# Performance work log

Measured on AMD Instinct MI355X. Metric: run time of the kernel, lower is better.

The kernel has to match this reference:

```python
import jax, jax.numpy as jnp
import numpy as np

N_HOSTS = 16
N_WINDOW = 3
GAT_IN = 3
D = 16          # d_model = gat_output_feats = n_hosts
NHEAD = 2
HD = D // NHEAD # 8
FF = 64
PROTO_DIM = 8
LATENT = N_HOSTS * D * N_WINDOW  # 768
LN_EPS = 1e-5


def _positional_encoding():
    pos = np.arange(N_WINDOW, dtype=np.float32)[:, None]
    div = np.exp(np.arange(0, D, 2, dtype=np.float32) * (-np.log(10000.0) / D))
    pe = np.zeros((N_WINDOW, D), dtype=np.float32)
    pe[:, 0::2] = np.sin(pos * div)
    pe[:, 1::2] = np.cos(pos * div)
    return jnp.asarray(pe[:, None, :])  # (n_window, 1, d_model)


def setup_inputs() -> dict:
    key = jax.random.key(0)
    ks = iter(jax.random.split(key, 40))
    p = lambda *s: jax.random.normal(next(ks), s, dtype=jnp.float32) * 0.05
    inp = {
        't': jax.random.normal(next(ks), (N_WINDOW * N_HOSTS * GAT_IN,), dtype=jnp.float32),
        's': jax.random.normal(next(ks), (N_HOSTS, PROTO_DIM), dtype=jnp.float32),
        # GAT (single head, fully connected 16-node graph)
        'gat_W': p(GAT_IN, D), 'gat_a_src': p(D), 'gat_a_dst': p(D),
        # time encoder Linear(16,16)
        'te_W': p(D, D), 'te_b': p(D),
        'pe': _positional_encoding(),
        # 2 transformer encoder layers, stacked on leading axis
        'qkv_W': p(2, 3 * D, D), 'qkv_b': p(2, 3 * D),
        'out_W': p(2, D, D), 'out_b': p(2, D),
        'ln1_g': jnp.ones((2, D), jnp.float32), 'ln1_b': jnp.zeros((2, D), jnp.float32),
        'ff1_W': p(2, FF, D), 'ff1_b': p(2, FF),
        'ff2_W': p(2, D, FF), 'ff2_b': p(2, D),
        'ln2_g': jnp.ones((2, D), jnp.float32), 'ln2_b': jnp.zeros((2, D), jnp.float32),
        # decoder heads
        'an_W': p(2 * N_HOSTS, LATENT), 'an_b': p(2 * N_HOSTS),
        'pr_W': p(PROTO_DIM * N_HOSTS, LATENT), 'pr_b': p(PROTO_DIM * N_HOSTS),
    }
    return inp


def _layer_norm(x, g, b):
    m = x.mean(-1, keepdims=True)
    v = ((x - m) ** 2).mean(-1, keepdims=True)
    return (x - m) * jax.lax.rsqrt(v + LN_EPS) * g + b


def reference(t, s, gat_W, gat_a_src, gat_a_dst, te_W, te_b, pe,
              qkv_W, qkv_b, out_W, out_b, ln1_g, ln1_b,
              ff1_W, ff1_b, ff2_W, ff2_b, ln2_g, ln2_b,
              an_W, an_b, pr_W, pr_b):
    # --- GAT over fully connected 16-host graph, per window ---
    x = t.reshape(N_WINDOW, N_HOSTS, GAT_IN)
    h = x @ gat_W                                   # (w, n, D)
    e_src = h @ gat_a_src                           # (w, n)
    e_dst = h @ gat_a_dst                           # (w, n)
    e = jax.nn.leaky_relu(e_src[:, :, None] + e_dst[:, None, :], 0.2)  # (w, src, dst)
    alpha = jax.nn.softmax(e, axis=1)               # softmax over sources, per dst
    gat_out = jax.nn.elu(jnp.einsum('wsd,wsf->wdf', alpha, h))         # (w, n, D)
    # --- time encode + positional encode (dropout = identity in eval) ---
    xe = gat_out @ te_W.T + te_b + pe               # (seq=3, batch=16, D)
    # --- 2 post-norm TransformerEncoderLayers ---
    inv_sqrt_hd = 1.0 / np.sqrt(HD).astype(np.float32)
    for l in range(2):
        qkv = xe @ qkv_W[l].T + qkv_b[l]            # (s, b, 3D)
        q, k, v = jnp.split(qkv, 3, axis=-1)
        hd = lambda z: z.reshape(N_WINDOW, N_HOSTS, NHEAD, HD).transpose(1, 2, 0, 3)  # (b,h,s,hd)
        q, k, v = hd(q), hd(k), hd(v)
        att = jax.nn.softmax(jnp.einsum('bhqd,bhkd->bhqk', q, k) * inv_sqrt_hd, axis=-1)
        ctx = jnp.einsum('bhqk,bhkd->bhqd', att, v).transpose(2, 0, 1, 3).reshape(N_WINDOW, N_HOSTS, D)
        xe = _layer_norm(xe + ctx @ out_W[l].T + out_b[l], ln1_g[l], ln1_b[l])
        ff = jax.nn.relu(xe @ ff1_W[l].T + ff1_b[l]) @ ff2_W[l].T + ff2_b[l]
        xe = _layer_norm(xe + ff, ln2_g[l], ln2_b[l])
    # --- flatten to latent (batch-major, matching permute(1,0,2).reshape) ---
    latent = xe.transpose(1, 0, 2).reshape(1, LATENT)
    # nn.LeakyReLU(True): negative_slope=True==1.0, i.e. identity (faithful to source)
    anomaly = jax.nn.leaky_relu(latent @ an_W.T + an_b, 1.0).reshape(N_HOSTS, 2)
    proto = jax.nn.sigmoid(latent @ pr_W.T + pr_b).reshape(N_HOSTS, PROTO_DIM)
    return anomaly, proto
```

## Files before the change

### kernel.cpp

```cpp
#include <hip/hip_runtime.h>
#include <hip/hip_bf16.h>


#define NW 3
#define NHOST 16
#define DM 16
#define FFD 64
#define LAT 768

typedef __hip_bfloat16 bf16;
typedef __attribute__((ext_vector_type(8))) unsigned short ushort8v;

static __device__ __forceinline__ float u2f(unsigned short u) {
    return __uint_as_float(((unsigned)u) << 16);
}

static __device__ __forceinline__ float lwf(const unsigned short* a, int i) { return u2f(a[i]); }
static __device__ __forceinline__ float lwf(const float* a, int i) { return a[i]; }

static __device__ __forceinline__ float gld(const bf16* p, int i) { return __bfloat162float(p[i]); }
static __device__ __forceinline__ float gld(const float* p, int i) { return p[i]; }
static __device__ __forceinline__ void gst(bf16* p, int i, float v) { p[i] = __float2bfloat16(v); }
static __device__ __forceinline__ void gst(float* p, int i, float v) { p[i] = v; }

enum {
    OFF_T    = 0,
    OFF_GATW = 144,
    OFF_ASRC = 192,
    OFF_ADST = 208,
    OFF_TEW  = 224,
    OFF_TEB  = 480,
    OFF_PE   = 496,
    OFF_QKVW = 544,
    OFF_QKVB = 2080,
    OFF_OUTW = 2176,
    OFF_OUTB = 2688,
    OFF_LN1G = 2720,
    OFF_LN1B = 2752,
    OFF_FF1W = 2784,
    OFF_FF1B = 4832,
    OFF_FF2W = 4960,
    OFF_FF2B = 7008,
    OFF_LN2G = 7040,
    OFF_LN2B = 7072,
    TOTAL_W  = 7104
};

struct Smem {
    float h[NW][NHOST][DM];
    float esrc[NW][NHOST];
    float edst[NW][NHOST];
    float alpha[NW][NHOST][NHOST];
    float xe[NW][NHOST][DM];
    float qkv[NW][NHOST][48];
    float ctx[NW][NHOST][DM];
    float tmp[NW][NHOST][DM];
    float ffh[NW][NHOST][FFD];
    float latent[LAT];
    float part[4];
};

template<typename T, typename WT>
__device__ void run_all(Smem& sm, WT* smW, int tid, int o,
    const T* t, const T* gat_W, const T* a_src, const T* a_dst,
    const T* te_W, const T* te_b, const T* pe,
    const T* qkv_W, const T* qkv_b, const T* out_W, const T* out_b,
    const T* ln1_g, const T* ln1_b,
    const T* ff1_W, const T* ff1_b, const T* ff2_W, const T* ff2_b,
    const T* ln2_g, const T* ln2_b,
    const T* an_W, const T* an_b, const T* pr_W, const T* pr_b,
    T* out)
{
    T wr0{}, wr1{}, wr2{}, wr3{};
    if (tid < 192) {
        const T* Wr = (o < 32) ? (an_W + o * LAT) : (pr_W + (o - 32) * LAT);
        wr0 = Wr[tid * 4];     wr1 = Wr[tid * 4 + 1];
        wr2 = Wr[tid * 4 + 2]; wr3 = Wr[tid * 4 + 3];
    }

    {
        constexpr int EPC = 16 / (int)sizeof(T);
        constexpr int NCHUNK = TOTAL_W / EPC;
        for (int g = tid; g < NCHUNK; g += 256) {
            int e = g * EPC;
            const T* p; int base;
            if      (e < OFF_GATW) { p = t;      base = OFF_T; }
            else if (e < OFF_ASRC) { p = gat_W;  base = OFF_GATW; }
            else if (e < OFF_ADST) { p = a_src;  base = OFF_ASRC; }
            else if (e < OFF_TEW)  { p = a_dst;  base = OFF_ADST; }
            else if (e < OFF_TEB)  { p = te_W;   base = OFF_TEW; }
            else if (e < OFF_PE)   { p = te_b;   base = OFF_TEB; }
            else if (e < OFF_QKVW) { p = pe;     base = OFF_PE; }
            else if (e < OFF_QKVB) { p = qkv_W;  base = OFF_QKVW; }
            else if (e < OFF_OUTW) { p = qkv_b;  base = OFF_QKVB; }
            else if (e < OFF_OUTB) { p = out_W;  base = OFF_OUTW; }
            else if (e < OFF_LN1G) { p = out_b;  base = OFF_OUTB; }
            else if (e < OFF_LN1B) { p = ln1_g;  base = OFF_LN1G; }
            else if (e < OFF_FF1W) { p = ln1_b;  base = OFF_LN1B; }
            else if (e < OFF_FF1B) { p = ff1_W;  base = OFF_FF1W; }
            else if (e < OFF_FF2W) { p = ff1_b;  base = OFF_FF1B; }
            else if (e < OFF_FF2B) { p = ff2_W;  base = OFF_FF2W; }
            else if (e < OFF_LN2G) { p = ff2_b;  base = OFF_FF2B; }
            else if (e < OFF_LN2B) { p = ln2_g;  base = OFF_LN2G; }
            else                   { p = ln2_b;  base = OFF_LN2B; }
            *(ushort8v*)((unsigned char*)smW + (size_t)e * sizeof(T)) =
                *(const ushort8v*)(p + (e - base));
        }
    }
    __syncthreads();

    for (int idx = tid; idx < NW * NHOST * DM; idx += 256) {
        int w = idx >> 8, r = idx & 255, n = r >> 4, f = r & 15;
        float acc = 0.f;
        #pragma unroll
        for (int i = 0; i < 3; ++i)
            acc += lwf(smW, OFF_T + (w * NHOST + n) * 3 + i) * lwf(smW, OFF_GATW + i * DM + f);
        sm.h[w][n][f] = acc;
    }
    __syncthreads();

    if (tid < 96) {
        int w = tid / 32, r = tid % 32, n = r & 15, which = r >> 4;
        int abase = which ? OFF_ADST : OFF_ASRC;
        float acc = 0.f;
        #pragma unroll
        for (int f = 0; f < DM; ++f) acc += sm.h[w][n][f] * lwf(smW, abase + f);
        if (which) sm.edst[w][n] = acc; else sm.esrc[w][n] = acc;
    }
    __syncthreads();

    if (tid < 48) {
        int w = tid / 16, d = tid & 15;
        float ed = sm.edst[w][d];
        float e[16];
        float mx = -1e30f;
        #pragma unroll
        for (int s = 0; s < 16; ++s) {
            float x = sm.esrc[w][s] + ed;
            x = x > 0.f ? x : 0.2f * x;
            e[s] = x;
            mx = fmaxf(mx, x);
        }
        float sum = 0.f;
        #pragma unroll
        for (int s = 0; s < 16; ++s) { e[s] = __expf(e[s] - mx); sum += e[s]; }
        float inv = 1.f / sum;
        #pragma unroll
        for (int s = 0; s < 16; ++s) sm.alpha[w][s][d] = e[s] * inv;
    }
    __syncthreads();

    for (int idx = tid; idx < NW * NHOST * DM; idx += 256) {
        int w = idx >> 8, r = idx & 255, d = r >> 4, f = r & 15;
        float acc = 0.f;
        #pragma unroll
        for (int s = 0; s < 16; ++s) acc += sm.alpha[w][s][d] * sm.h[w][s][f];
        sm.tmp[w][d][f] = acc > 0.f ? acc : (__expf(acc) - 1.f);
    }
    __syncthreads();

    for (int idx = tid; idx < NW * NHOST * DM; idx += 256) {
        int w = idx >> 8, r = idx & 255, n = r >> 4, f = r & 15;
        float acc = lwf(smW, OFF_TEB + f) + lwf(smW, OFF_PE + w * DM + f);
        #pragma unroll
        for (int g = 0; g < DM; ++g)
            acc += sm.tmp[w][n][g] * lwf(smW, OFF_TEW + f * DM + g);
        sm.xe[w][n][f] = acc;
    }
    __syncthreads();

    #pragma unroll 1
    for (int l = 0; l < 2; ++l) {
        int qW = OFF_QKVW + l * 768, qb = OFF_QKVB + l * 48;
        for (int idx = tid; idx < NW * NHOST * 48; idx += 256) {
            int w = idx / (NHOST * 48), r = idx % (NHOST * 48), n = r / 48, j = r % 48;
            float acc = lwf(smW, qb + j);
            #pragma unroll
            for (int f = 0; f < DM; ++f) acc += sm.xe[w][n][f] * lwf(smW, qW + j * DM + f);
            sm.qkv[w][n][j] = acc;
        }
        __syncthreads();

        if (tid < 96) {
            int b = tid / 6, r = tid % 6, hh = r / 3, qs = r % 3;
            const float inv_sqrt_hd = 0.35355339059327373f;
            float sc[3];
            #pragma unroll
            for (int ks = 0; ks < 3; ++ks) {
                float acc = 0.f;
                #pragma unroll
                for (int d0 = 0; d0 < 8; ++d0)
                    acc += sm.qkv[qs][b][hh * 8 + d0] * sm.qkv[ks][b][16 + hh * 8 + d0];
                sc[ks] = acc * inv_sqrt_hd;
            }
            float mx = fmaxf(sc[0], fmaxf(sc[1], sc[2]));
            float s0 = __expf(sc[0] - mx), s1 = __expf(sc[1] - mx), s2 = __expf(sc[2] - mx);
            float inv = 1.f / (s0 + s1 + s2);
            s0 *= inv; s1 *= inv; s2 *= inv;
            #pragma unroll
            for (int d0 = 0; d0 < 8; ++d0)
                sm.ctx[qs][b][hh * 8 + d0] = s0 * sm.qkv[0][b][32 + hh * 8 + d0]
                                           + s1 * sm.qkv[1][b][32 + hh * 8 + d0]
                                           + s2 * sm.qkv[2][b][32 + hh * 8 + d0];
        }
        __syncthreads();

        int oW = OFF_OUTW + l * 256, ob = OFF_OUTB + l * 16;
        for (int idx = tid; idx < NW * NHOST * DM; idx += 256) {
            int w = idx >> 8, r = idx & 255, n = r >> 4, f = r & 15;
            float acc = lwf(smW, ob + f) + sm.xe[w][n][f];
            #pragma unroll
            for (int g = 0; g < DM; ++g) acc += sm.ctx[w][n][g] * lwf(smW, oW + f * DM + g);
            sm.tmp[w][n][f] = acc;
        }
        __syncthreads();

        if (tid < 48) {
            int w = tid / 16, n = tid & 15;
            float m = 0.f;
            #pragma unroll
            for (int f = 0; f < DM; ++f) m += sm.tmp[w][n][f];
            m *= (1.f / 16.f);
            float v = 0.f;
            #pragma unroll
            for (int f = 0; f < DM; ++f) { float d0 = sm.tmp[w][n][f] - m; v += d0 * d0; }
            v *= (1.f / 16.f);
            float rr = rsqrtf(v + 1e-5f);
            #pragma unroll
            for (int f = 0; f < DM; ++f)
                sm.xe[w][n][f] = (sm.tmp[w][n][f] - m) * rr * lwf(smW, OFF_LN1G + l * DM + f)
                               + lwf(smW, OFF_LN1B + l * DM + f);
        }
        __syncthreads();

        int f1W = OFF_FF1W + l * 1024, f1b = OFF_FF1B + l * 64;
        for (int idx = tid; idx < NW * NHOST * FFD; idx += 256) {
            int w = idx / (NHOST * FFD), r = idx % (NHOST * FFD), n = r / FFD, j = r % FFD;
            float acc = lwf(smW, f1b + j);
            #pragma unroll
            for (int f = 0; f < DM; ++f) acc += sm.xe[w][n][f] * lwf(smW, f1W + j * DM + f);
            sm.ffh[w][n][j] = fmaxf(acc, 0.f);
        }
        __syncthreads();

        int f2W = OFF_FF2W + l * 1024, f2b = OFF_FF2B + l * 16;
        for (int idx = tid; idx < NW * NHOST * DM; idx += 256) {
            int w = idx >> 8, r = idx & 255, n = r >> 4, f = r & 15;
            float acc = lwf(smW, f2b + f) + sm.xe[w][n][f];
            #pragma unroll
            for (int j = 0; j < FFD; ++j) acc += sm.ffh[w][n][j] * lwf(smW, f2W + f * FFD + j);
            sm.tmp[w][n][f] = acc;
        }
        __syncthreads();

        if (tid < 48) {
            int w = tid / 16, n = tid & 15;
            float m = 0.f;
            #pragma unroll
            for (int f = 0; f < DM; ++f) m += sm.tmp[w][n][f];
            m *= (1.f / 16.f);
            float v = 0.f;
            #pragma unroll
            for (int f = 0; f < DM; ++f) { float d0 = sm.tmp[w][n][f] - m; v += d0 * d0; }
            v *= (1.f / 16.f);
            float rr = rsqrtf(v + 1e-5f);
            #pragma unroll
            for (int f = 0; f < DM; ++f)
                sm.xe[w][n][f] = (sm.tmp[w][n][f] - m) * rr * lwf(smW, OFF_LN2G + l * DM + f)
                               + lwf(smW, OFF_LN2B + l * DM + f);
        }
        __syncthreads();
    }

    for (int idx = tid; idx < LAT; idx += 256) {
        int w = idx >> 8, r = idx & 255, n = r >> 4, f = r & 15;
        sm.latent[n * 48 + w * DM + f] = sm.xe[w][n][f];
    }
    __syncthreads();

    float acc = 0.f;
    if (tid < 192) {
        int e0 = tid * 4;
        acc = sm.latent[e0]     * gld(&wr0, 0)
            + sm.latent[e0 + 1] * gld(&wr1, 0)
            + sm.latent[e0 + 2] * gld(&wr2, 0)
            + sm.latent[e0 + 3] * gld(&wr3, 0);
    }
    #pragma unroll
    for (int m = 1; m < 64; m <<= 1) acc += __shfl_xor(acc, m);
    if ((tid & 63) == 0) sm.part[tid >> 6] = acc;
    __syncthreads();
    if (tid == 0) {
        float s = sm.part[0] + sm.part[1] + sm.part[2] + sm.part[3];
        if (o < 32) {
            gst(out, o, s + gld(an_b, o));
        } else {
            float z = s + gld(pr_b, o - 32);
            gst(out, o, 1.f / (1.f + __expf(-z)));
        }
    }
}

__global__ void __launch_bounds__(256) txf_fused(
    const void* t, const void* gat_W, const void* a_src, const void* a_dst,
    const void* te_W, const void* te_b, const void* pe,
    const void* qkv_W, const void* qkv_b, const void* out_W, const void* out_b,
    const void* ln1_g, const void* ln1_b,
    const void* ff1_W, const void* ff1_b, const void* ff2_W, const void* ff2_b,
    const void* ln2_g, const void* ln2_b,
    const void* an_W, const void* an_b, const void* pr_W, const void* pr_b,
    void* out)
{
    __shared__ Smem sm;
    __shared__ __align__(16) unsigned char wbuf[TOTAL_W * 4];
    const int tid = threadIdx.x;
    const int o = blockIdx.x;
    unsigned w0 = *(const unsigned*)ln1_g;
    if (w0 == 0x3F803F80u) {
        run_all<bf16, unsigned short>(sm, (unsigned short*)wbuf, tid, o,
            (const bf16*)t, (const bf16*)gat_W, (const bf16*)a_src, (const bf16*)a_dst,
            (const bf16*)te_W, (const bf16*)te_b, (const bf16*)pe,
            (const bf16*)qkv_W, (const bf16*)qkv_b, (const bf16*)out_W, (const bf16*)out_b,
            (const bf16*)ln1_g, (const bf16*)ln1_b,
            (const bf16*)ff1_W, (const bf16*)ff1_b, (const bf16*)ff2_W, (const bf16*)ff2_b,
            (const bf16*)ln2_g, (const bf16*)ln2_b,
            (const bf16*)an_W, (const bf16*)an_b, (const bf16*)pr_W, (const bf16*)pr_b,
            (bf16*)out);
    } else {
        run_all<float, float>(sm, (float*)wbuf, tid, o,
            (const float*)t, (const float*)gat_W, (const float*)a_src, (const float*)a_dst,
            (const float*)te_W, (const float*)te_b, (const float*)pe,
            (const float*)qkv_W, (const float*)qkv_b, (const float*)out_W, (const float*)out_b,
            (const float*)ln1_g, (const float*)ln1_b,
            (const float*)ff1_W, (const float*)ff1_b, (const float*)ff2_W, (const float*)ff2_b,
            (const float*)ln2_g, (const float*)ln2_b,
            (const float*)an_W, (const float*)an_b, (const float*)pr_W, (const float*)pr_b,
            (float*)out);
    }
}

extern "C" void kernel_launch(void* const* d_in, const int* in_sizes, int n_in,
                              void* d_out, int out_size, void* d_ws, size_t ws_size,
                              hipStream_t stream) {
    txf_fused<<<160, 256, 0, stream>>>(
        d_in[0],
        d_in[2], d_in[3], d_in[4],
        d_in[5], d_in[6], d_in[7],
        d_in[8], d_in[9], d_in[10], d_in[11],
        d_in[12], d_in[13],
        d_in[14], d_in[15], d_in[16], d_in[17],
        d_in[18], d_in[19],
        d_in[20], d_in[21], d_in[22], d_in[23],
        d_out);
}
```

Baseline: 127.0 us.

## Fuse GAT and transformer stages into row-per-thread passes with fewer barriers

Merges the GAT projection and attention-score steps, folds the softmax aggregation, ELU and time-encoder into one per-row pass, and fuses multi-head attention with the output projection and first LayerNorm. The final LayerNorm now writes the latent layout directly, so the separate transpose pass is gone. Shared-memory accesses switch to vectorized float4 and 8-wide weight loads, and the alpha and ctx buffers are removed. The goal is fewer __syncthreads barriers and less shared-memory traffic on a latency-bound single-block pipeline, at the cost of running fused stages on only 48 or 192 threads, which reduces parallelism and raises register pressure.

```diff
diff --git a/kernel.cpp b/kernel.cpp
--- a/kernel.cpp
+++ b/kernel.cpp
@@ -17,6 +17,36 @@
 
 static __device__ __forceinline__ float lwf(const unsigned short* a, int i) { return u2f(a[i]); }
 static __device__ __forceinline__ float lwf(const float* a, int i) { return a[i]; }
+
+static __device__ __forceinline__ void wld8(const unsigned short* a, int off, float* o) {
+    ushort8v v = *(const ushort8v*)(a + off);
+    #pragma unroll
+    for (int u = 0; u < 8; ++u) o[u] = u2f(v[u]);
+}
+static __device__ __forceinline__ void wld8(const float* a, int off, float* o) {
+    float4 x = *(const float4*)(a + off);
+    float4 y = *(const float4*)(a + off + 4);
+    o[0]=x.x; o[1]=x.y; o[2]=x.z; o[3]=x.w; o[4]=y.x; o[5]=y.y; o[6]=y.z; o[7]=y.w;
+}
+template<typename WT>
+static __device__ __forceinline__ void wld16(const WT* a, int off, float* o) {
+    wld8(a, off, o); wld8(a, off + 8, o + 8);
+}
+
+static __device__ __forceinline__ void ldrow8(const float* p, float* o) {
+    float4 x = ((const float4*)p)[0], y = ((const float4*)p)[1];
+    o[0]=x.x; o[1]=x.y; o[2]=x.z; o[3]=x.w; o[4]=y.x; o[5]=y.y; o[6]=y.z; o[7]=y.w;
+}
+static __device__ __forceinline__ void ldrow16(const float* p, float* o) {
+    ldrow8(p, o); ldrow8(p + 8, o + 8);
+}
+static __device__ __forceinline__ void strow16(float* p, const float* o) {
+    #pragma unroll
+    for (int c = 0; c < 4; ++c) {
+        float4 v = { o[c*4+0], o[c*4+1], o[c*4+2], o[c*4+3] };
+        ((float4*)p)[c] = v;
+    }
+}
 
 static __device__ __forceinline__ float gld(const bf16* p, int i) { return __bfloat162float(p[i]); }
 static __device__ __forceinline__ float gld(const float* p, int i) { return p[i]; }
@@ -46,14 +76,12 @@
     TOTAL_W  = 7104
 };
 
-struct Smem {
+struct __align__(16) Smem {
     float h[NW][NHOST][DM];
     float esrc[NW][NHOST];
     float edst[NW][NHOST];
-    float alpha[NW][NHOST][NHOST];
     float xe[NW][NHOST][DM];
     float qkv[NW][NHOST][48];
-    float ctx[NW][NHOST][DM];
     float tmp[NW][NHOST][DM];
     float ffh[NW][NHOST][FFD];
     float latent[LAT];
@@ -109,174 +137,217 @@
     }
     __syncthreads();
 
-    for (int idx = tid; idx < NW * NHOST * DM; idx += 256) {
-        int w = idx >> 8, r = idx & 255, n = r >> 4, f = r & 15;
-        float acc = 0.f;
-        #pragma unroll
-        for (int i = 0; i < 3; ++i)
-            acc += lwf(smW, OFF_T + (w * NHOST + n) * 3 + i) * lwf(smW, OFF_GATW + i * DM + f);
-        sm.h[w][n][f] = acc;
-    }
-    __syncthreads();
-
-    if (tid < 96) {
-        int w = tid / 32, r = tid % 32, n = r & 15, which = r >> 4;
-        int abase = which ? OFF_ADST : OFF_ASRC;
-        float acc = 0.f;
-        #pragma unroll
-        for (int f = 0; f < DM; ++f) acc += sm.h[w][n][f] * lwf(smW, abase + f);
-        if (which) sm.edst[w][n] = acc; else sm.esrc[w][n] = acc;
+    if (tid < 48) {
+        int w = tid / 16, n = tid & 15;
+        float x0 = lwf(smW, OFF_T + (w * NHOST + n) * 3 + 0);
+        float x1 = lwf(smW, OFF_T + (w * NHOST + n) * 3 + 1);
+        float x2 = lwf(smW, OFF_T + (w * NHOST + n) * 3 + 2);
+        float g0[16], g1[16], g2[16];
+        wld16(smW, OFF_GATW, g0);
+        wld16(smW, OFF_GATW + 16, g1);
+        wld16(smW, OFF_GATW + 32, g2);
+        float hr[16];
+        #pragma unroll
+        for (int f = 0; f < 16; ++f) hr[f] = x0 * g0[f] + x1 * g1[f] + x2 * g2[f];
+        strow16(sm.h[w][n], hr);
+        float as[16], ad[16];
+        wld16(smW, OFF_ASRC, as);
+        wld16(smW, OFF_ADST, ad);
+        float es = 0.f, ed = 0.f;
+        #pragma unroll
+        for (int f = 0; f < 16; ++f) { es += hr[f] * as[f]; ed += hr[f] * ad[f]; }
+        sm.esrc[w][n] = es; sm.edst[w][n] = ed;
     }
     __syncthreads();
 
     if (tid < 48) {
         int w = tid / 16, d = tid & 15;
         float ed = sm.edst[w][d];
-        float e[16];
-        float mx = -1e30f;
+        float er[16]; ldrow16(sm.esrc[w], er);
+        float e[16], mx = -1e30f;
         #pragma unroll
         for (int s = 0; s < 16; ++s) {
-            float x = sm.esrc[w][s] + ed;
+            float x = er[s] + ed;
             x = x > 0.f ? x : 0.2f * x;
-            e[s] = x;
-            mx = fmaxf(mx, x);
+            e[s] = x; mx = fmaxf(mx, x);
         }
         float sum = 0.f;
         #pragma unroll
         for (int s = 0; s < 16; ++s) { e[s] = __expf(e[s] - mx); sum += e[s]; }
         float inv = 1.f / sum;
-        #pragma unroll
-        for (int s = 0; s < 16; ++s) sm.alpha[w][s][d] = e[s] * inv;
-    }
-    __syncthreads();
-
-    for (int idx = tid; idx < NW * NHOST * DM; idx += 256) {
-        int w = idx >> 8, r = idx & 255, d = r >> 4, f = r & 15;
-        float acc = 0.f;
-        #pragma unroll
-        for (int s = 0; s < 16; ++s) acc += sm.alpha[w][s][d] * sm.h[w][s][f];
-        sm.tmp[w][d][f] = acc > 0.f ? acc : (__expf(acc) - 1.f);
-    }
-    __syncthreads();
-
-    for (int idx = tid; idx < NW * NHOST * DM; idx += 256) {
-        int w = idx >> 8, r = idx & 255, n = r >> 4, f = r & 15;
-        float acc = lwf(smW, OFF_TEB + f) + lwf(smW, OFF_PE + w * DM + f);
-        #pragma unroll
-        for (int g = 0; g < DM; ++g)
-            acc += sm.tmp[w][n][g] * lwf(smW, OFF_TEW + f * DM + g);
-        sm.xe[w][n][f] = acc;
+        float row[16];
+        #pragma unroll
+        for (int f = 0; f < 16; ++f) row[f] = 0.f;
+        #pragma unroll
+        for (int s = 0; s < 16; ++s) {
+            float a = e[s] * inv;
+            float hs[16]; ldrow16(sm.h[w][s], hs);
+            #pragma unroll
+            for (int f = 0; f < 16; ++f) row[f] += a * hs[f];
+        }
+        #pragma unroll
+        for (int f = 0; f < 16; ++f)
+            row[f] = row[f] > 0.f ? row[f] : (__expf(row[f]) - 1.f);
+        float xr[16];
+        #pragma unroll
+        for (int f = 0; f < 16; ++f) {
+            float wv[16]; wld16(smW, OFF_TEW + f * 16, wv);
+            float acc = lwf(smW, OFF_TEB + f) + lwf(smW, OFF_PE + w * 16 + f);
+            #pragma unroll
+            for (int g = 0; g < 16; ++g) acc += row[g] * wv[g];
+            xr[f] = acc;
+        }
+        strow16(sm.xe[w][d], xr);
     }
     __syncthreads();
 
     #pragma unroll 1
     for (int l = 0; l < 2; ++l) {
-        int qW = OFF_QKVW + l * 768, qb = OFF_QKVB + l * 48;
-        for (int idx = tid; idx < NW * NHOST * 48; idx += 256) {
-            int w = idx / (NHOST * 48), r = idx % (NHOST * 48), n = r / 48, j = r % 48;
-            float acc = lwf(smW, qb + j);
-            #pragma unroll
-            for (int f = 0; f < DM; ++f) acc += sm.xe[w][n][f] * lwf(smW, qW + j * DM + f);
-            sm.qkv[w][n][j] = acc;
+        const int qW = OFF_QKVW + l * 768, qb = OFF_QKVB + l * 48;
+        const int oW = OFF_OUTW + l * 256, ob = OFF_OUTB + l * 16;
+        const int f1W = OFF_FF1W + l * 1024, f1b = OFF_FF1B + l * 64;
+        const int f2W = OFF_FF2W + l * 1024, f2b = OFF_FF2B + l * 16;
+
+        if (tid < 192) {
+            int r = tid >> 2, q = tid & 3;
+            int w = r / 16, n = r & 15;
+            float x[16]; ldrow16(sm.xe[w][n], x);
+            int j0 = q * 12;
+            #pragma unroll
+            for (int j = j0; j < j0 + 12; ++j) {
+                float wv[16]; wld16(smW, qW + j * 16, wv);
+                float acc = lwf(smW, qb + j);
+                #pragma unroll
+                for (int g = 0; g < 16; ++g) acc += x[g] * wv[g];
+                sm.qkv[w][n][j] = acc;
+            }
         }
         __syncthreads();
 
-        if (tid < 96) {
-            int b = tid / 6, r = tid % 6, hh = r / 3, qs = r % 3;
-            const float inv_sqrt_hd = 0.35355339059327373f;
-            float sc[3];
-            #pragma unroll
-            for (int ks = 0; ks < 3; ++ks) {
-                float acc = 0.f;
-                #pragma unroll
-                for (int d0 = 0; d0 < 8; ++d0)
-                    acc += sm.qkv[qs][b][hh * 8 + d0] * sm.qkv[ks][b][16 + hh * 8 + d0];
-                sc[ks] = acc * inv_sqrt_hd;
+        if (tid < 48) {
+            int b = tid / 3, qs = tid - 3 * b;
+            const float isq = 0.35355339059327373f;
+            float ctxr[16];
+            #pragma unroll
+            for (int hh = 0; hh < 2; ++hh) {
+                float qh[8]; ldrow8(&sm.qkv[qs][b][hh * 8], qh);
+                float sc[3];
+                #pragma unroll
+                for (int ks = 0; ks < 3; ++ks) {
+                    float kh[8]; ldrow8(&sm.qkv[ks][b][16 + hh * 8], kh);
+                    float acc = 0.f;
+                    #pragma unroll
+                    for (int dd = 0; dd < 8; ++dd) acc += qh[dd] * kh[dd];
+                    sc[ks] = acc * isq;
+                }
+                float mx = fmaxf(sc[0], fmaxf(sc[1], sc[2]));
+                float s0 = __expf(sc[0] - mx), s1 = __expf(sc[1] - mx), s2 = __expf(sc[2] - mx);
+                float inv = 1.f / (s0 + s1 + s2);
+                s0 *= inv; s1 *= inv; s2 *= inv;
+                #pragma unroll
+                for (int dd = 0; dd < 8; ++dd) ctxr[hh * 8 + dd] = 0.f;
+                float vh[8];
+                ldrow8(&sm.qkv[0][b][32 + hh * 8], vh);
+                #pragma unroll
+                for (int dd = 0; dd < 8; ++dd) ctxr[hh * 8 + dd] += s0 * vh[dd];
+                ldrow8(&sm.qkv[1][b][32 + hh * 8], vh);
+                #pragma unroll
+                for (int dd = 0; dd < 8; ++dd) ctxr[hh * 8 + dd] += s1 * vh[dd];
+                ldrow8(&sm.qkv[2][b][32 + hh * 8], vh);
+                #pragma unroll
+                for (int dd = 0; dd < 8; ++dd) ctxr[hh * 8 + dd] += s2 * vh[dd];
             }
-            float mx = fmaxf(sc[0], fmaxf(sc[1], sc[2]));
-            float s0 = __expf(sc[0] - mx), s1 = __expf(sc[1] - mx), s2 = __expf(sc[2] - mx);
-            float inv = 1.f / (s0 + s1 + s2);
-            s0 *= inv; s1 *= inv; s2 *= inv;
-            #pragma unroll
-            for (int d0 = 0; d0 < 8; ++d0)
-                sm.ctx[qs][b][hh * 8 + d0] = s0 * sm.qkv[0][b][32 + hh * 8 + d0]
-                                           + s1 * sm.qkv[1][b][32 + hh * 8 + d0]
-                                           + s2 * sm.qkv[2][b][32 + hh * 8 + d0];
+            float xr[16]; ldrow16(sm.xe[qs][b], xr);
+            float tr[16];
+            #pragma unroll
+            for (int f = 0; f < 16; ++f) {
+                float wv[16]; wld16(smW, oW + f * 16, wv);
+                float acc = lwf(smW, ob + f) + xr[f];
+                #pragma unroll
+                for (int g = 0; g < 16; ++g) acc += ctxr[g] * wv[g];
+                tr[f] = acc;
+            }
+            float m = 0.f;
+            #pragma unroll
+            for (int f = 0; f < 16; ++f) m += tr[f];
+            m *= (1.f / 16.f);
+            float v = 0.f;
+            #pragma unroll
+            for (int f = 0; f < 16; ++f) { float d0 = tr[f] - m; v += d0 * d0; }
+            float rr = rsqrtf(v * (1.f / 16.f) + 1e-5f);
+            float g16[16], b16[16];
+            wld16(smW, OFF_LN1G + l * 16, g16);
+            wld16(smW, OFF_LN1B + l * 16, b16);
+            float xo[16];
+            #pragma unroll
+            for (int f = 0; f < 16; ++f) xo[f] = (tr[f] - m) * rr * g16[f] + b16[f];
+            strow16(sm.xe[qs][b], xo);
         }
         __syncthreads();
 
-        int oW = OFF_OUTW + l * 256, ob = OFF_OUTB + l * 16;
-        for (int idx = tid; idx < NW * NHOST * DM; idx += 256) {
-            int w = idx >> 8, r = idx & 255, n = r >> 4, f = r & 15;
-            float acc = lwf(smW, ob + f) + sm.xe[w][n][f];
-            #pragma unroll
-            for (int g = 0; g < DM; ++g) acc += sm.ctx[w][n][g] * lwf(smW, oW + f * DM + g);
-            sm.tmp[w][n][f] = acc;
+        if (tid < 192) {
+            int r = tid >> 2, q = tid & 3;
+            int w = r / 16, n = r & 15;
+            float x[16]; ldrow16(sm.xe[w][n], x);
+            int j0 = q * 16;
+            float fr[16];
+            #pragma unroll
+            for (int jj = 0; jj < 16; ++jj) {
+                int j = j0 + jj;
+                float wv[16]; wld16(smW, f1W + j * 16, wv);
+                float acc = lwf(smW, f1b + j);
+                #pragma unroll
+                for (int g = 0; g < 16; ++g) acc += x[g] * wv[g];
+                fr[jj] = fmaxf(acc, 0.f);
+            }
+            strow16(&sm.ffh[w][n][j0], fr);
+        }
+        __syncthreads();
+
+        if (tid < 192) {
+            int r = tid >> 2, q = tid & 3;
+            int w = r / 16, n = r & 15;
+            float xr[64];
+            #pragma unroll
+            for (int c = 0; c < 4; ++c) ldrow16(&sm.ffh[w][n][c * 16], &xr[c * 16]);
+            int f0 = q * 4;
+            #pragma unroll
+            for (int ff = 0; ff < 4; ++ff) {
+                int f = f0 + ff;
+                float acc = lwf(smW, f2b + f) + sm.xe[w][n][f];
+                #pragma unroll
+                for (int c = 0; c < 8; ++c) {
+                    float wv[8]; wld8(smW, f2W + f * 64 + c * 8, wv);
+                    #pragma unroll
+                    for (int u = 0; u < 8; ++u) acc += xr[c * 8 + u] * wv[u];
+                }
+                sm.tmp[w][n][f] = acc;
+            }
         }
         __syncthreads();
 
         if (tid < 48) {
             int w = tid / 16, n = tid & 15;
+            float tr[16]; ldrow16(sm.tmp[w][n], tr);
             float m = 0.f;
             #pragma unroll
-            for (int f = 0; f < DM; ++f) m += sm.tmp[w][n][f];
+            for (int f = 0; f < 16; ++f) m += tr[f];
             m *= (1.f / 16.f);
             float v = 0.f;
             #pragma unroll
-            for (int f = 0; f < DM; ++f) { float d0 = sm.tmp[w][n][f] - m; v += d0 * d0; }
-            v *= (1.f / 16.f);
-            float rr = rsqrtf(v + 1e-5f);
-            #pragma unroll
-            for (int f = 0; f < DM; ++f)
-                sm.xe[w][n][f] = (sm.tmp[w][n][f] - m) * rr * lwf(smW, OFF_LN1G + l * DM + f)
-                               + lwf(smW, OFF_LN1B + l * DM + f);
+            for (int f = 0; f < 16; ++f) { float d0 = tr[f] - m; v += d0 * d0; }
+            float rr = rsqrtf(v * (1.f / 16.f) + 1e-5f);
+            float g16[16], b16[16];
+            wld16(smW, OFF_LN2G + l * 16, g16);
+            wld16(smW, OFF_LN2B + l * 16, b16);
+            float xo[16];
+            #pragma unroll
+            for (int f = 0; f < 16; ++f) xo[f] = (tr[f] - m) * rr * g16[f] + b16[f];
+            if (l == 0) strow16(sm.xe[w][n], xo);
+            else        strow16(&sm.latent[n * 48 + w * 16], xo);
         }
         __syncthreads();
-
-        int f1W = OFF_FF1W + l * 1024, f1b = OFF_FF1B + l * 64;
-        for (int idx = tid; idx < NW * NHOST * FFD; idx += 256) {
-            int w = idx / (NHOST * FFD), r = idx % (NHOST * FFD), n = r / FFD, j = r % FFD;
-            float acc = lwf(smW, f1b + j);
-            #pragma unroll
-            for (int f = 0; f < DM; ++f) acc += sm.xe[w][n][f] * lwf(smW, f1W + j * DM + f);
-            sm.ffh[w][n][j] = fmaxf(acc, 0.f);
-        }
-        __syncthreads();
-
-        int f2W = OFF_FF2W + l * 1024, f2b = OFF_FF2B + l * 16;
-        for (int idx = tid; idx < NW * NHOST * DM; idx += 256) {
-            int w = idx >> 8, r = idx & 255, n = r >> 4, f = r & 15;
-            float acc = lwf(smW, f2b + f) + sm.xe[w][n][f];
-            #pragma unroll
-            for (int j = 0; j < FFD; ++j) acc += sm.ffh[w][n][j] * lwf(smW, f2W + f * FFD + j);
-            sm.tmp[w][n][f] = acc;
-        }
-        __syncthreads();
-
-        if (tid < 48) {
-            int w = tid / 16, n = tid & 15;
-            float m = 0.f;
-            #pragma unroll
-            for (int f = 0; f < DM; ++f) m += sm.tmp[w][n][f];
-            m *= (1.f / 16.f);
-            float v = 0.f;
-            #pragma unroll
-            for (int f = 0; f < DM; ++f) { float d0 = sm.tmp[w][n][f] - m; v += d0 * d0; }
-            v *= (1.f / 16.f);
-            float rr = rsqrtf(v + 1e-5f);
-            #pragma unroll
-            for (int f = 0; f < DM; ++f)
-                sm.xe[w][n][f] = (sm.tmp[w][n][f] - m) * rr * lwf(smW, OFF_LN2G + l * DM + f)
-                               + lwf(smW, OFF_LN2B + l * DM + f);
-        }
-        __syncthreads();
-    }
-
-    for (int idx = tid; idx < LAT; idx += 256) {
-        int w = idx >> 8, r = idx & 255, n = r >> 4, f = r & 15;
-        sm.latent[n * 48 + w * DM + f] = sm.xe[w][n][f];
-    }
-    __syncthreads();
+    }
 
     float acc = 0.f;
     if (tid < 192) {
```

Result: faster. 124.2 us (-2.2%).
